# Optimization experiments

Measured on AMD Instinct MI355X. Metric: run time of the kernel, lower is better.

The kernel has to match this reference:

```python
import jax, jax.numpy as jnp
import numpy as np

V, D, S, H, B = 32000, 1024, 2048, 16, 4
DFF = 4 * D
HD = D // H
EPS = 1e-5


def _layernorm(x, g, b):
    mu = jnp.mean(x, axis=-1, keepdims=True)
    var = jnp.var(x, axis=-1, keepdims=True)
    return (x - mu) * jax.lax.rsqrt(var + EPS) * g + b


def setup_inputs() -> dict:
    key = jax.random.key(0)
    ks = jax.random.split(key, 14)
    s = 0.02
    return {
        "tokens": jax.random.randint(ks[0], (B, S), 0, V),
        "emb": jax.random.normal(ks[1], (V, D), jnp.float32) * s,
        "pos": jax.random.normal(ks[2], (1, S, D), jnp.float32) * s,
        "w_qkv": jax.random.normal(ks[3], (3 * D, D), jnp.float32) * s,
        "b_qkv": jnp.zeros((3 * D,), jnp.float32),
        "w_o": jax.random.normal(ks[4], (D, D), jnp.float32) * s,
        "b_o": jnp.zeros((D,), jnp.float32),
        "g1": jnp.ones((D,), jnp.float32),
        "beta1": jnp.zeros((D,), jnp.float32),
        "w1": jax.random.normal(ks[5], (DFF, D), jnp.float32) * s,
        "b1": jnp.zeros((DFF,), jnp.float32),
        "w2": jax.random.normal(ks[6], (D, DFF), jnp.float32) * s,
        "b2": jnp.zeros((D,), jnp.float32),
        "g2": jnp.ones((D,), jnp.float32),
        "beta2": jnp.zeros((D,), jnp.float32),
        "w_fc": jax.random.normal(ks[7], (V, D), jnp.float32) * s,
        "b_fc": jnp.zeros((V,), jnp.float32),
    }


def reference(tokens, emb, pos, w_qkv, b_qkv, w_o, b_o, g1, beta1, w1, b1,
              w2, b2, g2, beta2, w_fc, b_fc):
    # embedding + learned positional embedding: [B, S, D]
    x = emb[tokens] + pos
    # multi-head self-attention (torch nn.MultiheadAttention semantics)
    qkv = jnp.einsum('bsd,ed->bse', x, w_qkv) + b_qkv
    q, k, v = jnp.split(qkv, 3, axis=-1)
    q = q.reshape(B, S, H, HD)
    k = k.reshape(B, S, H, HD)
    v = v.reshape(B, S, H, HD)
    scores = jnp.einsum('bqhd,bkhd->bhqk', q, k) / jnp.sqrt(jnp.float32(HD))
    attn = jax.nn.softmax(scores, axis=-1)
    ctx = jnp.einsum('bhqk,bkhd->bqhd', attn, v).reshape(B, S, D)
    attn_out = jnp.einsum('bsd,ed->bse', ctx, w_o) + b_o
    # residual + norm1
    x = _layernorm(x + attn_out, g1, beta1)
    # FFN with ReLU (the custom_relu is mathematically plain ReLU)
    h = jnp.maximum(jnp.einsum('bsd,fd->bsf', x, w1) + b1, 0.0)
    ffn = jnp.einsum('bsf,df->bsd', h, w2) + b2
    # residual + norm2
    x = _layernorm(x + ffn, g2, beta2)
    # final vocab projection
    logits = jnp.einsum('bsd,vd->bsv', x, w_fc) + b_fc
    return logits
```

## Files before the change

### kernel.cpp

```cpp
#include <hip/hip_runtime.h>
#include <stdint.h>

#define Bz   4
#define Sq   2048
#define Dm   1024
#define Hh   16
#define HDm  64
#define DFFm 4096
#define Vv   32000
#define MTOK (Bz * Sq)

typedef unsigned short u16;
typedef __attribute__((ext_vector_type(8))) short short8v;
typedef __attribute__((ext_vector_type(4))) float f32x4;

struct alignas(8) U16x4 { u16 x, y, z, w; };

typedef const __attribute__((address_space(1))) void* gptr1_t;
typedef __attribute__((address_space(3))) void* lptr3_t;

__device__ __forceinline__ u16 f2bf(float f) {
    union { float f; unsigned u; } v; v.f = f;
    unsigned r = v.u + 0x7FFF + ((v.u >> 16) & 1);
    return (u16)(r >> 16);
}
__device__ __forceinline__ float bf2f(u16 h) {
    union { unsigned u; float f; } v; v.u = ((unsigned)h) << 16;
    return v.f;
}

#define WAITVM(N) asm volatile("s_waitcnt vmcnt(" #N ")" ::: "memory")

__device__ __forceinline__ void barrier_fenced() {
    asm volatile("" ::: "memory");
    __builtin_amdgcn_s_barrier();
    asm volatile("" ::: "memory");
}

__global__ void to_bf16(const float* __restrict__ in, u16* __restrict__ out, long n4) {
    long i = (long)blockIdx.x * blockDim.x + threadIdx.x;
    const long stride = (long)gridDim.x * blockDim.x;
    for (; i < n4; i += stride) {
        float4 v = *(const float4*)(in + i * 4);
        U16x4 h = { f2bf(v.x), f2bf(v.y), f2bf(v.z), f2bf(v.w) };
        *(U16x4*)(out + i * 4) = h;
    }
}

__global__ void embed_kernel(const int* __restrict__ tok, const float* __restrict__ emb,
                             const float* __restrict__ pos, float* __restrict__ x32,
                             u16* __restrict__ x16) {
    const int row = blockIdx.x;
    const int s = row & (Sq - 1);
    const int t = threadIdx.x;
    const long tokid = tok[row];
    float4 e = *(const float4*)(emb + tokid * Dm + t * 4);
    float4 p = *(const float4*)(pos + (long)s * Dm + t * 4);
    float4 v = { e.x + p.x, e.y + p.y, e.z + p.z, e.w + p.w };
    const long base = (long)row * Dm + t * 4;
    *(float4*)(x32 + base) = v;
    U16x4 h = { f2bf(v.x), f2bf(v.y), f2bf(v.z), f2bf(v.w) };
    *(U16x4*)(x16 + base) = h;
}

template <int OUTMODE, int RELU>
__global__ __launch_bounds__(256) void gemm128(
    const u16* __restrict__ A, const u16* __restrict__ B,
    const float* __restrict__ bias, void* __restrict__ Cp,
    int M, int N, int K, float alpha)
{
    __shared__ u16 smem[24576];

    const int bid = blockIdx.x;
    const int mtiles = M >> 7;
    const int mpx = mtiles >> 3;
    const int x   = bid & 7;
    const int loc = bid >> 3;
    const int im  = x * mpx + (loc % mpx);
    const int in  = loc / mpx;
    const int row0 = im * 128, col0 = in * 128;

    const int t = threadIdx.x;
    const int lane = t & 63;
    const int wid = t >> 6;
    const int wr = (wid >> 1) * 64;
    const int wc = (wid & 1) * 64;
    const int fr = lane & 15;
    const int g4 = lane >> 4;

    f32x4 acc[4][4];
#pragma unroll
    for (int m = 0; m < 4; ++m)
#pragma unroll
        for (int n = 0; n < 4; ++n) acc[m][n] = f32x4{0.f, 0.f, 0.f, 0.f};

    const int nt = K >> 5;

    auto stage = [&](const u16* __restrict__ g, int rowbase, u16* dst) {
#pragma unroll
        for (int j = 0; j < 2; ++j) {
            const int slot = j * 256 + t;
            const int row = slot >> 2;
            const int c8 = (slot & 3) ^ ((row >> 1) & 3);
            const u16* sp = g + (long)(rowbase + row) * K + c8 * 8;
            __builtin_amdgcn_global_load_lds((gptr1_t)sp,
                (lptr3_t)(dst + slot * 8), 16, 0, 0);
        }
    };

    auto rdT = [&](const u16* base, int rbase) -> short8v {
        const int r = rbase + fr;
        return *(const short8v*)(base + r * 32 + ((g4 ^ ((r >> 1) & 3)) << 3));
    };

    stage(A, row0, smem);
    stage(B, col0, smem + 12288);
    if (nt > 1) {
        stage(A + 32, row0, smem + 4096);
        stage(B + 32, col0, smem + 12288 + 4096);
        WAITVM(4);
    } else {
        WAITVM(0);
    }
    barrier_fenced();

    short8v fa[4], fb[4];

    for (int tt = 0; tt < nt; ++tt) {
        u16* rA = smem + ((unsigned)tt % 3u) * 4096;
        u16* rB = smem + 12288 + ((unsigned)tt % 3u) * 4096;
        u16* sA = smem + ((unsigned)(tt + 2) % 3u) * 4096;
        u16* sB = smem + 12288 + ((unsigned)(tt + 2) % 3u) * 4096;

#pragma unroll
        for (int m = 0; m < 4; ++m) fa[m] = rdT(rA, wr + m * 16);
#pragma unroll
        for (int n = 0; n < 4; ++n) fb[n] = rdT(rB, wc + n * 16);

        if (tt + 2 < nt) {
            stage(A + (tt + 2) * 32, row0, sA);
            stage(B + (tt + 2) * 32, col0, sB);
            WAITVM(4);
        } else {
            WAITVM(0);
        }
        barrier_fenced();
        asm volatile("s_waitcnt lgkmcnt(0)" ::: "memory");
        __builtin_amdgcn_s_setprio(1);
#pragma unroll
        for (int m = 0; m < 4; ++m)
#pragma unroll
            for (int n = 0; n < 4; ++n)
                acc[m][n] = __builtin_amdgcn_mfma_f32_16x16x32_bf16(fa[m], fb[n], acc[m][n], 0, 0, 0);
        __builtin_amdgcn_s_setprio(0);
        barrier_fenced();
    }

    const int rq = (lane >> 4) * 4;
    float bv[4];
#pragma unroll
    for (int n = 0; n < 4; ++n)
        bv[n] = bias ? bias[col0 + wc + n * 16 + fr] : 0.f;
#pragma unroll
    for (int m = 0; m < 4; ++m) {
#pragma unroll
        for (int n = 0; n < 4; ++n) {
            const int col = col0 + wc + n * 16 + fr;
#pragma unroll
            for (int r = 0; r < 4; ++r) {
                const int row = row0 + wr + m * 16 + rq + r;
                float v = alpha * acc[m][n][r] + bv[n];
                if (RELU) v = fmaxf(v, 0.f);
                if (OUTMODE == 0)
                    ((float*)Cp)[(long)row * N + col] = v;
                else
                    ((u16*)Cp)[(long)row * N + col] = f2bf(v);
            }
        }
    }
}

__global__ void transpose_v(const u16* __restrict__ qkv, u16* __restrict__ vt) {
    const int kt = blockIdx.x * 64;
    const int bh = blockIdx.y;
    const int b = bh >> 4, h = bh & 15;
    const int t = threadIdx.x;
    __shared__ u16 tile[64][72];
    const long src = (long)b * Sq * (3 * Dm) + 2 * Dm + h * HDm;
#pragma unroll
    for (int i = 0; i < 2; ++i) {
        const int kl = i * 32 + (t >> 3);
        const int d0 = (t & 7) * 8;
        short8v v = *(const short8v*)(qkv + src + (long)(kt + kl) * (3 * Dm) + d0);
        *(short8v*)(&tile[kl][d0]) = v;
    }
    __syncthreads();
#pragma unroll
    for (int i = 0; i < 2; ++i) {
        const int d = i * 32 + (t >> 3);
        const int kk0 = (t & 7) * 8;
        short8v o;
#pragma unroll
        for (int j = 0; j < 8; ++j) o[j] = (short)tile[kk0 + j][d];
        *(short8v*)(vt + ((long)bh * HDm + d) * Sq + kt + kk0) = o;
    }
}

__global__ __launch_bounds__(256) void flash_attn(
    const u16* __restrict__ qkv, const u16* __restrict__ vt,
    u16* __restrict__ ctx)
{
    __shared__ u16 Kt[2][64 * 64];
    __shared__ u16 Vt[2][64 * 64];
    __shared__ u16 Pt[4][32 * 64];

    const int bh = blockIdx.y;
    const int b = bh >> 4, h = bh & 15;
    const int t = threadIdx.x;
    const int lane = t & 63;
    const int wid = t >> 6;
    const int fr = lane & 15;
    const int g = lane >> 4;
    const int qb = blockIdx.x * 128 + wid * 32;

    short8v aq[2][2];
#pragma unroll
    for (int qn = 0; qn < 2; ++qn)
#pragma unroll
        for (int kk = 0; kk < 2; ++kk) {
            const long q = (long)b * Sq + qb + qn * 16 + fr;
            aq[qn][kk] = *(const short8v*)(qkv + q * (3 * Dm) + h * 64 + kk * 32 + g * 8);
        }

    const int srl = t >> 3;
    const int sc8 = t & 7;
    const long kbase = (long)b * Sq * (3 * Dm) + Dm + h * 64;
    const long vbase = (long)bh * HDm * Sq;

    auto stage = [&](int kt, int buf) {
#pragma unroll
        for (int j = 0; j < 2; ++j) {
            const int rl = srl + j * 32;
            const int c8 = sc8 ^ (rl & 7);
            const u16* ks = qkv + kbase + (long)(kt * 64 + rl) * (3 * Dm) + c8 * 8;
            __builtin_amdgcn_global_load_lds((gptr1_t)ks,
                (lptr3_t)(&Kt[buf][rl * 64 + sc8 * 8]), 16, 0, 0);
            const u16* vs = vt + vbase + (long)rl * Sq + kt * 64 + c8 * 8;
            __builtin_amdgcn_global_load_lds((gptr1_t)vs,
                (lptr3_t)(&Vt[buf][rl * 64 + sc8 * 8]), 16, 0, 0);
        }
    };

    f32x4 accO[4][2];
#pragma unroll
    for (int dm = 0; dm < 4; ++dm)
#pragma unroll
        for (int qn = 0; qn < 2; ++qn) accO[dm][qn] = f32x4{0.f, 0.f, 0.f, 0.f};
    float m0 = -3.0e38f, m1 = -3.0e38f, l0 = 0.f, l1 = 0.f;
    const float cl2 = 0.125f * 1.44269504f;

    stage(0, 0);
    WAITVM(0);
    barrier_fenced();

    for (int kt = 0; kt < Sq / 64; ++kt) {
        const int cur = kt & 1;
        if (kt + 1 < Sq / 64) stage(kt + 1, cur ^ 1);

        f32x4 s[4][2];
#pragma unroll
        for (int kvm = 0; kvm < 4; ++kvm)
#pragma unroll
            for (int qn = 0; qn < 2; ++qn) s[kvm][qn] = f32x4{0.f, 0.f, 0.f, 0.f};
        __builtin_amdgcn_s_setprio(1);
#pragma unroll
        for (int kvm = 0; kvm < 4; ++kvm)
#pragma unroll
            for (int kk = 0; kk < 2; ++kk) {
                const int r = kvm * 16 + fr;
                short8v bk = *(const short8v*)(&Kt[cur][r * 64 + (((kk * 4 + g) ^ (r & 7)) << 3)]);
#pragma unroll
                for (int qn = 0; qn < 2; ++qn)
                    s[kvm][qn] = __builtin_amdgcn_mfma_f32_16x16x32_bf16(bk, aq[qn][kk], s[kvm][qn], 0, 0, 0);
            }
        __builtin_amdgcn_s_setprio(0);

        float t0 = -3.0e38f, t1 = -3.0e38f;
#pragma unroll
        for (int kvm = 0; kvm < 4; ++kvm)
#pragma unroll
            for (int r = 0; r < 4; ++r) {
                t0 = fmaxf(t0, s[kvm][0][r]);
                t1 = fmaxf(t1, s[kvm][1][r]);
            }
        t0 = fmaxf(t0, __shfl_xor(t0, 16)); t0 = fmaxf(t0, __shfl_xor(t0, 32));
        t1 = fmaxf(t1, __shfl_xor(t1, 16)); t1 = fmaxf(t1, __shfl_xor(t1, 32));
        const float mn0 = fmaxf(m0, t0 * cl2);
        const float mn1 = fmaxf(m1, t1 * cl2);
        const float a0 = __builtin_amdgcn_exp2f(m0 - mn0);
        const float a1 = __builtin_amdgcn_exp2f(m1 - mn1);
        m0 = mn0; m1 = mn1;

        float ps0 = 0.f, ps1 = 0.f;
#pragma unroll
        for (int kvm = 0; kvm < 4; ++kvm)
#pragma unroll
            for (int r = 0; r < 4; ++r) {
                float p0 = __builtin_amdgcn_exp2f(s[kvm][0][r] * cl2 - mn0);
                float p1 = __builtin_amdgcn_exp2f(s[kvm][1][r] * cl2 - mn1);
                s[kvm][0][r] = p0; ps0 += p0;
                s[kvm][1][r] = p1; ps1 += p1;
            }
        ps0 += __shfl_xor(ps0, 16); ps0 += __shfl_xor(ps0, 32);
        ps1 += __shfl_xor(ps1, 16); ps1 += __shfl_xor(ps1, 32);
        l0 = l0 * a0 + ps0;
        l1 = l1 * a1 + ps1;
#pragma unroll
        for (int dm = 0; dm < 4; ++dm)
#pragma unroll
            for (int r = 0; r < 4; ++r) {
                accO[dm][0][r] *= a0;
                accO[dm][1][r] *= a1;
            }

#pragma unroll
        for (int kvm = 0; kvm < 4; ++kvm)
#pragma unroll
            for (int qn = 0; qn < 2; ++qn) {
                U16x4 hh = { f2bf(s[kvm][qn][0]), f2bf(s[kvm][qn][1]),
                             f2bf(s[kvm][qn][2]), f2bf(s[kvm][qn][3]) };
                const int q = qn * 16 + fr;
                const int off = q * 64 + (((2 * kvm + (g >> 1)) ^ (fr & 7)) << 3) + (g & 1) * 4;
                *(U16x4*)(&Pt[wid][off]) = hh;
            }
        short8v pb[2][2];
        short8v va[4][2];
#pragma unroll
        for (int qn = 0; qn < 2; ++qn)
#pragma unroll
            for (int ks = 0; ks < 2; ++ks) {
                const int q = qn * 16 + fr;
                pb[qn][ks] = *(const short8v*)(&Pt[wid][q * 64 + (((ks * 4 + g) ^ (fr & 7)) << 3)]);
            }
#pragma unroll
        for (int dm = 0; dm < 4; ++dm)
#pragma unroll
            for (int ks = 0; ks < 2; ++ks) {
                const int r = dm * 16 + fr;
                va[dm][ks] = *(const short8v*)(&Vt[cur][r * 64 + (((ks * 4 + g) ^ (r & 7)) << 3)]);
            }

        __builtin_amdgcn_s_setprio(1);
#pragma unroll
        for (int dm = 0; dm < 4; ++dm)
#pragma unroll
            for (int qn = 0; qn < 2; ++qn)
#pragma unroll
                for (int ks = 0; ks < 2; ++ks)
                    accO[dm][qn] = __builtin_amdgcn_mfma_f32_16x16x32_bf16(va[dm][ks], pb[qn][ks], accO[dm][qn], 0, 0, 0);
        __builtin_amdgcn_s_setprio(0);

        WAITVM(0);
        barrier_fenced();
    }

    const float inv0 = 1.f / l0;
    const float inv1 = 1.f / l1;
#pragma unroll
    for (int dm = 0; dm < 4; ++dm)
#pragma unroll
        for (int qn = 0; qn < 2; ++qn) {
            const float inv = qn ? inv1 : inv0;
            U16x4 hh = { f2bf(accO[dm][qn][0] * inv), f2bf(accO[dm][qn][1] * inv),
                         f2bf(accO[dm][qn][2] * inv), f2bf(accO[dm][qn][3] * inv) };
            const long q = (long)b * Sq + qb + qn * 16 + fr;
            *(U16x4*)(ctx + q * Dm + h * 64 + dm * 16 + g * 4) = hh;
        }
}

template <int W32>
__global__ void ln_kernel(float* __restrict__ x, const float* __restrict__ res,
                          const float* __restrict__ g, const float* __restrict__ be,
                          u16* __restrict__ out16) {
    const int row = blockIdx.x;
    const int t = threadIdx.x;
    const long base = (long)row * Dm + t * 4;
    float4 a = *(const float4*)(x + base);
    float4 b = *(const float4*)(res + base);
    float v0 = a.x + b.x, v1 = a.y + b.y, v2 = a.z + b.z, v3 = a.w + b.w;
    float s = v0 + v1 + v2 + v3;
    float q = v0 * v0 + v1 * v1 + v2 * v2 + v3 * v3;

    const int wave = t >> 6, lane = t & 63;
    __shared__ float rs[4], rq2[4];
#pragma unroll
    for (int o = 32; o; o >>= 1) { s += __shfl_xor(s, o); q += __shfl_xor(q, o); }
    if (lane == 0) { rs[wave] = s; rq2[wave] = q; }
    __syncthreads();
    s = rs[0] + rs[1] + rs[2] + rs[3];
    q = rq2[0] + rq2[1] + rq2[2] + rq2[3];

    const float mean = s * (1.f / Dm);
    const float var = q * (1.f / Dm) - mean * mean;
    const float rstd = rsqrtf(var + 1e-5f);
    const float4 gg = *(const float4*)(g + t * 4);
    const float4 bb = *(const float4*)(be + t * 4);
    float o0 = (v0 - mean) * rstd * gg.x + bb.x;
    float o1 = (v1 - mean) * rstd * gg.y + bb.y;
    float o2 = (v2 - mean) * rstd * gg.z + bb.z;
    float o3 = (v3 - mean) * rstd * gg.w + bb.w;
    U16x4 h = { f2bf(o0), f2bf(o1), f2bf(o2), f2bf(o3) };
    *(U16x4*)(out16 + base) = h;
    if (W32) {
        float4 ov = { o0, o1, o2, o3 };
        *(float4*)(x + base) = ov;
    }
}

extern "C" void kernel_launch(void* const* d_in, const int* in_sizes, int n_in,
                              void* d_out, int out_size, void* d_ws, size_t ws_size,
                              hipStream_t stream) {
    const int*   tokens = (const int*)  d_in[0];
    const float* emb    = (const float*)d_in[1];
    const float* pos    = (const float*)d_in[2];
    const float* w_qkv  = (const float*)d_in[3];
    const float* b_qkv  = (const float*)d_in[4];
    const float* w_o    = (const float*)d_in[5];
    const float* b_o    = (const float*)d_in[6];
    const float* g1     = (const float*)d_in[7];
    const float* beta1  = (const float*)d_in[8];
    const float* w1     = (const float*)d_in[9];
    const float* b1     = (const float*)d_in[10];
    const float* w2     = (const float*)d_in[11];
    const float* b2     = (const float*)d_in[12];
    const float* g2     = (const float*)d_in[13];
    const float* beta2  = (const float*)d_in[14];
    const float* w_fc   = (const float*)d_in[15];
    const float* b_fc   = (const float*)d_in[16];

    char* ws = (char*)d_ws;
    size_t off = 0;
    auto alloc = [&](size_t bytes) { void* p = ws + off; off += (bytes + 255) & ~(size_t)255; return p; };

    float* X32   = (float*)alloc((size_t)MTOK * Dm * 4);
    u16*   XB16  = (u16*)  alloc((size_t)MTOK * Dm * 2);
    u16*   QKV16 = (u16*)  alloc((size_t)MTOK * 3 * Dm * 2);
    u16*   VT16  = (u16*)  alloc((size_t)64 * HDm * Sq * 2);
    u16*   CTX16 = (u16*)  alloc((size_t)MTOK * Dm * 2);
    float* ATT32 = (float*)alloc((size_t)MTOK * Dm * 4);
    u16*   H16   = (u16*)  alloc((size_t)MTOK * DFFm * 2);
    u16*   WQ16  = (u16*)  alloc((size_t)3 * Dm * Dm * 2);
    u16*   WO16  = (u16*)  alloc((size_t)Dm * Dm * 2);
    u16*   W116  = (u16*)  alloc((size_t)DFFm * Dm * 2);
    u16*   W216  = (u16*)  alloc((size_t)Dm * DFFm * 2);
    u16*   WFC16 = (u16*)  alloc((size_t)Vv * Dm * 2);

    const dim3 blk(256);

    to_bf16<<<1024, blk, 0, stream>>>(w_qkv, WQ16, (long)3 * Dm * Dm / 4);
    to_bf16<<<1024, blk, 0, stream>>>(w_o,   WO16, (long)Dm * Dm / 4);
    to_bf16<<<1024, blk, 0, stream>>>(w1,    W116, (long)DFFm * Dm / 4);
    to_bf16<<<1024, blk, 0, stream>>>(w2,    W216, (long)Dm * DFFm / 4);
    to_bf16<<<2048, blk, 0, stream>>>(w_fc,  WFC16, (long)Vv * Dm / 4);

    embed_kernel<<<MTOK, blk, 0, stream>>>(tokens, emb, pos, X32, XB16);

    gemm128<1, 0><<<dim3((MTOK / 128) * ((3 * Dm) / 128)), blk, 0, stream>>>(
        XB16, WQ16, b_qkv, QKV16, MTOK, 3 * Dm, Dm, 1.f);

    transpose_v<<<dim3(Sq / 64, Bz * Hh), blk, 0, stream>>>(QKV16, VT16);

    flash_attn<<<dim3(Sq / 128, Bz * Hh), blk, 0, stream>>>(QKV16, VT16, CTX16);

    gemm128<0, 0><<<dim3((MTOK / 128) * (Dm / 128)), blk, 0, stream>>>(
        CTX16, WO16, b_o, ATT32, MTOK, Dm, Dm, 1.f);

    ln_kernel<1><<<MTOK, blk, 0, stream>>>(X32, ATT32, g1, beta1, XB16);

    gemm128<1, 1><<<dim3((MTOK / 128) * (DFFm / 128)), blk, 0, stream>>>(
        XB16, W116, b1, H16, MTOK, DFFm, Dm, 1.f);

    gemm128<0, 0><<<dim3((MTOK / 128) * (Dm / 128)), blk, 0, stream>>>(
        H16, W216, b2, ATT32, MTOK, Dm, DFFm, 1.f);

    ln_kernel<0><<<MTOK, blk, 0, stream>>>(X32, ATT32, g2, beta2, XB16);

    gemm128<0, 0><<<dim3((MTOK / 128) * (Vv / 128)), blk, 0, stream>>>(
        XB16, WFC16, b_fc, (float*)d_out, MTOK, Vv, Dm, 1.f);
}
```

Baseline: 1.282 ms.

## Switch GEMMs to 256x256 tiles with 512 threads and split-phase pipelining

Replaces the 128x128, 256-thread GEMM with a 256x256 tile run by 8 waves, each computing a 128x64 sub-tile. The K loop is split into two MFMA phases per step, one per half of the wave's A rows. A uses a 3-deep LDS ring and B a 5-deep ring, so B is prefetched four steps ahead and A two steps ahead. The goal is more arithmetic per LDS and global byte loaded, and better latency hiding. The cost is 128KB of LDS, one block per CU, twice as many barriers per K step, and coarser tiles that leave fewer blocks for the smaller GEMMs.

```diff
diff --git a/kernel.cpp b/kernel.cpp
--- a/kernel.cpp
+++ b/kernel.cpp
@@ -64,42 +64,45 @@
 }
 
 template <int OUTMODE, int RELU>
-__global__ __launch_bounds__(256) void gemm128(
+__global__ __launch_bounds__(512, 1) void gemm_dp(
     const u16* __restrict__ A, const u16* __restrict__ B,
     const float* __restrict__ bias, void* __restrict__ Cp,
     int M, int N, int K, float alpha)
 {
-    __shared__ u16 smem[24576];
+    __shared__ u16 smem[65536];
 
     const int bid = blockIdx.x;
-    const int mtiles = M >> 7;
+    const int mtiles = M >> 8;
     const int mpx = mtiles >> 3;
     const int x   = bid & 7;
     const int loc = bid >> 3;
     const int im  = x * mpx + (loc % mpx);
     const int in  = loc / mpx;
-    const int row0 = im * 128, col0 = in * 128;
+    const int row0 = im * 256, col0 = in * 256;
 
     const int t = threadIdx.x;
     const int lane = t & 63;
     const int wid = t >> 6;
-    const int wr = (wid >> 1) * 64;
-    const int wc = (wid & 1) * 64;
+    const int wm = (wid >> 2) * 128;
+    const int wn = (wid & 3) * 64;
     const int fr = lane & 15;
     const int g4 = lane >> 4;
 
-    f32x4 acc[4][4];
-#pragma unroll
-    for (int m = 0; m < 4; ++m)
+    f32x4 acc[8][4];
+#pragma unroll
+    for (int m = 0; m < 8; ++m)
 #pragma unroll
         for (int n = 0; n < 4; ++n) acc[m][n] = f32x4{0.f, 0.f, 0.f, 0.f};
 
     const int nt = K >> 5;
 
+    auto Ab = [&](int i) -> u16* { return smem + i * 8192; };
+    auto Bb = [&](int i) -> u16* { return smem + 24576 + i * 8192; };
+
     auto stage = [&](const u16* __restrict__ g, int rowbase, u16* dst) {
 #pragma unroll
         for (int j = 0; j < 2; ++j) {
-            const int slot = j * 256 + t;
+            const int slot = j * 512 + t;
             const int row = slot >> 2;
             const int c8 = (slot & 3) ^ ((row >> 1) & 3);
             const u16* sp = g + (long)(rowbase + row) * K + c8 * 8;
@@ -113,34 +116,42 @@
         return *(const short8v*)(base + r * 32 + ((g4 ^ ((r >> 1) & 3)) << 3));
     };
 
-    stage(A, row0, smem);
-    stage(B, col0, smem + 12288);
-    if (nt > 1) {
-        stage(A + 32, row0, smem + 4096);
-        stage(B + 32, col0, smem + 12288 + 4096);
-        WAITVM(4);
-    } else {
-        WAITVM(0);
-    }
+    stage(A,          row0, Ab(0));
+    stage(B,          col0, Bb(0));
+    stage(A + 32,     row0, Ab(1));
+    stage(B + 32,     col0, Bb(1));
+    stage(B + 64,     col0, Bb(2));
+    stage(B + 96,     col0, Bb(3));
+    WAITVM(8);
     barrier_fenced();
 
-    short8v fa[4], fb[4];
+    short8v fa[4], fa2[4], fb[4];
 
     for (int tt = 0; tt < nt; ++tt) {
-        u16* rA = smem + ((unsigned)tt % 3u) * 4096;
-        u16* rB = smem + 12288 + ((unsigned)tt % 3u) * 4096;
-        u16* sA = smem + ((unsigned)(tt + 2) % 3u) * 4096;
-        u16* sB = smem + 12288 + ((unsigned)(tt + 2) % 3u) * 4096;
-
-#pragma unroll
-        for (int m = 0; m < 4; ++m) fa[m] = rdT(rA, wr + m * 16);
-#pragma unroll
-        for (int n = 0; n < 4; ++n) fb[n] = rdT(rB, wc + n * 16);
-
-        if (tt + 2 < nt) {
-            stage(A + (tt + 2) * 32, row0, sA);
-            stage(B + (tt + 2) * 32, col0, sB);
-            WAITVM(4);
+        u16* rA = Ab((unsigned)tt % 3u);
+        u16* rB = Bb((unsigned)tt % 5u);
+
+#pragma unroll
+        for (int m = 0; m < 4; ++m) fa[m] = rdT(rA, wm + m * 16);
+#pragma unroll
+        for (int n = 0; n < 4; ++n) fb[n] = rdT(rB, wn + n * 16);
+        if (tt + 2 < nt) stage(A + (tt + 2) * 32, row0, Ab((unsigned)(tt + 2) % 3u));
+        barrier_fenced();
+        asm volatile("s_waitcnt lgkmcnt(0)" ::: "memory");
+        __builtin_amdgcn_s_setprio(1);
+#pragma unroll
+        for (int m = 0; m < 4; ++m)
+#pragma unroll
+            for (int n = 0; n < 4; ++n)
+                acc[m][n] = __builtin_amdgcn_mfma_f32_16x16x32_bf16(fa[m], fb[n], acc[m][n], 0, 0, 0);
+        __builtin_amdgcn_s_setprio(0);
+        barrier_fenced();
+
+#pragma unroll
+        for (int m = 0; m < 4; ++m) fa2[m] = rdT(rA, wm + 64 + m * 16);
+        if (tt + 4 < nt) {
+            stage(B + (tt + 4) * 32, col0, Bb((unsigned)(tt + 4) % 5u));
+            WAITVM(6);
         } else {
             WAITVM(0);
         }
@@ -151,7 +162,7 @@
         for (int m = 0; m < 4; ++m)
 #pragma unroll
             for (int n = 0; n < 4; ++n)
-                acc[m][n] = __builtin_amdgcn_mfma_f32_16x16x32_bf16(fa[m], fb[n], acc[m][n], 0, 0, 0);
+                acc[4 + m][n] = __builtin_amdgcn_mfma_f32_16x16x32_bf16(fa2[m], fb[n], acc[4 + m][n], 0, 0, 0);
         __builtin_amdgcn_s_setprio(0);
         barrier_fenced();
     }
@@ -160,15 +171,15 @@
     float bv[4];
 #pragma unroll
     for (int n = 0; n < 4; ++n)
-        bv[n] = bias ? bias[col0 + wc + n * 16 + fr] : 0.f;
-#pragma unroll
-    for (int m = 0; m < 4; ++m) {
+        bv[n] = bias ? bias[col0 + wn + n * 16 + fr] : 0.f;
+#pragma unroll
+    for (int m = 0; m < 8; ++m) {
 #pragma unroll
         for (int n = 0; n < 4; ++n) {
-            const int col = col0 + wc + n * 16 + fr;
+            const int col = col0 + wn + n * 16 + fr;
 #pragma unroll
             for (int r = 0; r < 4; ++r) {
-                const int row = row0 + wr + m * 16 + rq + r;
+                const int row = row0 + wm + m * 16 + rq + r;
                 float v = alpha * acc[m][n][r] + bv[n];
                 if (RELU) v = fmaxf(v, 0.f);
                 if (OUTMODE == 0)
@@ -456,6 +467,7 @@
     u16*   WFC16 = (u16*)  alloc((size_t)Vv * Dm * 2);
 
     const dim3 blk(256);
+    const dim3 blk512(512);
 
     to_bf16<<<1024, blk, 0, stream>>>(w_qkv, WQ16, (long)3 * Dm * Dm / 4);
     to_bf16<<<1024, blk, 0, stream>>>(w_o,   WO16, (long)Dm * Dm / 4);
@@ -465,26 +477,26 @@
 
     embed_kernel<<<MTOK, blk, 0, stream>>>(tokens, emb, pos, X32, XB16);
 
-    gemm128<1, 0><<<dim3((MTOK / 128) * ((3 * Dm) / 128)), blk, 0, stream>>>(
+    gemm_dp<1, 0><<<dim3((MTOK / 256) * ((3 * Dm) / 256)), blk512, 0, stream>>>(
         XB16, WQ16, b_qkv, QKV16, MTOK, 3 * Dm, Dm, 1.f);
 
     transpose_v<<<dim3(Sq / 64, Bz * Hh), blk, 0, stream>>>(QKV16, VT16);
 
     flash_attn<<<dim3(Sq / 128, Bz * Hh), blk, 0, stream>>>(QKV16, VT16, CTX16);
 
-    gemm128<0, 0><<<dim3((MTOK / 128) * (Dm / 128)), blk, 0, stream>>>(
+    gemm_dp<0, 0><<<dim3((MTOK / 256) * (Dm / 256)), blk512, 0, stream>>>(
         CTX16, WO16, b_o, ATT32, MTOK, Dm, Dm, 1.f);
 
     ln_kernel<1><<<MTOK, blk, 0, stream>>>(X32, ATT32, g1, beta1, XB16);
 
-    gemm128<1, 1><<<dim3((MTOK / 128) * (DFFm / 128)), blk, 0, stream>>>(
+    gemm_dp<1, 1><<<dim3((MTOK / 256) * (DFFm / 256)), blk512, 0, stream>>>(
         XB16, W116, b1, H16, MTOK, DFFm, Dm, 1.f);
 
-    gemm128<0, 0><<<dim3((MTOK / 128) * (Dm / 128)), blk, 0, stream>>>(
+    gemm_dp<0, 0><<<dim3((MTOK / 256) * (Dm / 256)), blk512, 0, stream>>>(
         H16, W216, b2, ATT32, MTOK, Dm, DFFm, 1.f);
 
     ln_kernel<0><<<MTOK, blk, 0, stream>>>(X32, ATT32, g2, beta2, XB16);
 
-    gemm128<0, 0><<<dim3((MTOK / 128) * (Vv / 128)), blk, 0, stream>>>(
+    gemm_dp<0, 0><<<dim3((MTOK / 256) * (Vv / 256)), blk512, 0, stream>>>(
         XB16, WFC16, b_fc, (float*)d_out, MTOK, Vv, Dm, 1.f);
 }
```

Result: faster. 1.197 ms (-6.6%).
